# Performance work log

Hardware: AMD Instinct MI355X
Metric: run time of the kernel (lower is better)

Reference implementation:

```python
import jax, jax.numpy as jnp
import numpy as np

B, T, E, H = 16, 4096, 64, 8
K, GADD, RADD, REGION = 256, 8, 8, 64
MIN_SIGMA, SIGMA_SCALE, SIGMA_BOOST = 0.05, 1.0, 2.0
VS = K * (4 + GADD + RADD)


def setup_inputs() -> dict:
    key = jax.random.key(0)
    ks = jax.random.split(key, 10)
    return {
        "x": jax.random.normal(ks[0], (B, T, E), jnp.float32),
        "Wq": jax.random.normal(ks[1], (E, E * H), jnp.float32) / np.float32(np.sqrt(E)),
        "Wk": jax.random.normal(ks[2], (E, E * H), jnp.float32) / np.float32(np.sqrt(E)),
        "Wv": jax.random.normal(ks[3], (E, E * H), jnp.float32) / np.float32(np.sqrt(E)),
        "Wu": jax.random.normal(ks[4], (H * E, E), jnp.float32) / np.float32(np.sqrt(H * E)),
        "bu": jnp.zeros((E,), jnp.float32),
        "means_p": jax.random.normal(ks[5], (K, 2), jnp.float32),
        "sigmas_p": jax.random.normal(ks[6], (K,), jnp.float32),
        "global_ints": jax.random.randint(ks[7], (B, 1, K, GADD, 2), 0, T, jnp.int32),
        "local_offsets": jax.random.randint(ks[8], (B, 1, K, RADD, 2), 0, REGION, jnp.int32),
    }


def _flip(x):
    # util.flip: sort each (i, j) pair so row >= col (below-diagonal / causal)
    hi = jnp.max(x, axis=-1, keepdims=True)
    lo = jnp.min(x, axis=-1, keepdims=True)
    return jnp.concatenate([hi, lo], axis=-1)


def _forward(x, Wq, Wk, Wv, Wu, bu, means_p, sigmas_p, global_ints, local_offsets):
    b, t, e = x.shape
    h, k = H, K

    # ---- hyper(): continuous means/sigmas over the (t, t) attention matrix
    means = jnp.broadcast_to(means_p[None, None], (b, 1, k, 2))
    means = _flip(means)
    means = jax.nn.sigmoid(means) * (t - 1)                       # (b,1,k,2) in [0, t-1]
    sig = jax.nn.softplus(sigmas_p + SIGMA_BOOST) + MIN_SIGMA     # (k,)
    sigmas = jnp.broadcast_to((sig * t * SIGMA_SCALE)[None, None, :, None], (b, 1, k, 2))

    # ---- ngenerate: 2^rank floor/ceil neighbours + global + relative-window samples
    fl, ce = jnp.floor(means), jnp.ceil(means)
    pat = jnp.array([[0., 0.], [0., 1.], [1., 0.], [1., 1.]], jnp.float32)  # (4,2)
    neigh = fl[:, :, :, None, :] * (1.0 - pat) + ce[:, :, :, None, :] * pat
    neigh = jnp.clip(neigh, 0, t - 1).astype(jnp.int32)           # (b,1,k,4,2)
    lower = jnp.clip(jnp.floor(means) - REGION // 2, 0, t - REGION).astype(jnp.int32)
    local = lower[:, :, :, None, :] + local_offsets               # (b,1,k,RADD,2)
    idx = jnp.concatenate([neigh, global_ints, local], axis=3).reshape(b, 1, VS, 2)
    idx = _flip(idx)                                              # (b,1,VS,2), row >= col

    # ---- densities: unnormalized Gaussian weight of each int tuple under each point
    indfl = idx.astype(jnp.float32)
    diff = (indfl[:, :, :, None, :] - means[:, :, None, :, :]) / sigmas[:, :, None, :, :]
    props = jnp.exp(-0.5 * jnp.sum(diff * diff, axis=-1))         # (b,1,VS,K)

    # ---- nduplicates: zero all-but-one of identical index tuples per batch
    ids = idx[:, 0, :, 0] * t + idx[:, 0, :, 1]                   # (b, VS)
    def dupmask(v):
        o = jnp.argsort(v)
        s = v[o]
        d = jnp.concatenate([jnp.zeros((1,), bool), s[1:] == s[:-1]])
        return jnp.zeros((VS,), bool).at[o].set(d)
    dups = jax.vmap(dupmask)(ids)                                  # (b, VS)
    props = jnp.where(dups[:, None, :, None], 0.0, props)
    props = props / jnp.sum(props, axis=2, keepdims=True)
    weights = jnp.sum(props, axis=3)                               # mvalues == 1 -> (b,1,VS)

    # ---- Q/K/V projections, per-head dim = e
    scale = e ** -0.25
    q = (x @ Wq).reshape(b, t, h, e).transpose(0, 2, 1, 3).reshape(b * h, t, e) * scale
    kk = (x @ Wk).reshape(b, t, h, e).transpose(0, 2, 1, 3).reshape(b * h, t, e) * scale
    v = (x @ Wv).reshape(b, t, h, e).transpose(0, 2, 1, 3).reshape(b * h, t, e)

    rows = jnp.broadcast_to(idx[:, 0, None, :, 0], (b, h, VS)).reshape(b * h, VS)
    cols = jnp.broadcast_to(idx[:, 0, None, :, 1], (b, h, VS)).reshape(b * h, VS)
    w = jnp.broadcast_to(weights[:, 0, None, :], (b, h, VS)).reshape(b * h, VS)

    sq = jnp.take_along_axis(q, rows[:, :, None], axis=1)          # (b*h, VS, e)
    sk = jnp.take_along_axis(kk, cols[:, :, None], axis=1)
    dot = w * jnp.sum(sq * sk, axis=-1)                            # (b*h, VS)

    # ---- segment (row-wise) softmax over the sparse pattern
    seg = (jnp.arange(b * h, dtype=jnp.int32)[:, None] * t + rows).reshape(-1)
    dflat = dot.reshape(-1)
    m = jax.lax.stop_gradient(jax.ops.segment_max(dflat, seg, num_segments=b * h * t))
    ex = jnp.exp(dflat - m[seg])
    ssum = jax.ops.segment_sum(ex, seg, num_segments=b * h * t)
    p = ex / ssum[seg]                                             # (b*h*VS,)

    # ---- sparse batched matmul: scatter-add p * V[col] into rows
    gathered = jnp.take_along_axis(v, cols[:, :, None], axis=1).reshape(-1, e)
    out = jax.ops.segment_sum(p[:, None] * gathered, seg, num_segments=b * h * t)
    out = out.reshape(b, h, t, e).transpose(0, 2, 1, 3).reshape(b, t, h * e)
    return out @ Wu + bu


def reference(x, Wq, Wk, Wv, Wu, bu, means_p, sigmas_p, global_ints, local_offsets):
    return _forward(x, Wq, Wk, Wv, Wu, bu, means_p, sigmas_p, global_ints, local_offsets)
```

## Files before the change

### kernel.cpp

```cpp
#include <hip/hip_runtime.h>
#include <hip/hip_bf16.h>
#include <math.h>

#define B 16
#define T 4096
#define E 64
#define H 8
#define KP 256
#define GADD 8
#define RADD 8
#define REGION 64
#define VS (KP * (4 + GADD + RADD))
#define NH (H * E)
#define NCHUNK 20
#define HSZ 16384

typedef __attribute__((ext_vector_type(8))) short bf16x8;
typedef __attribute__((ext_vector_type(4))) float f32x4;

__device__ inline ushort f2bf(float f) {
    union { __hip_bfloat16 h; ushort u; } cv;
    cv.h = __float2bfloat16(f);
    return cv.u;
}
__device__ inline float bflo(uint32_t p) { return __uint_as_float(p << 16); }
__device__ inline float bfhi(uint32_t p) { return __uint_as_float(p & 0xffff0000u); }

__global__ void k_points(const float* __restrict__ means_p, const float* __restrict__ sigmas_p,
                         float* __restrict__ meansf, float* __restrict__ sigt) {
    int k = threadIdx.x;
    if (k >= KP) return;
    float a = means_p[2 * k], b = means_p[2 * k + 1];
    float hi = fmaxf(a, b), lo = fminf(a, b);
    meansf[2 * k]     = (1.f / (1.f + expf(-hi))) * (float)(T - 1);
    meansf[2 * k + 1] = (1.f / (1.f + expf(-lo))) * (float)(T - 1);
    float sp = sigmas_p[k] + 2.0f;
    float s = (sp > 20.f) ? sp : log1pf(expf(sp));
    sigt[k] = (s + 0.05f) * (float)T;
}

__global__ void k_wvu(const float* __restrict__ Wv, const float* __restrict__ Wu,
                      float* __restrict__ Wvu) {
    int idx = blockIdx.x * blockDim.x + threadIdx.x;
    if (idx >= E * NH) return;
    int i = idx / NH, c = idx % NH;
    int h = c / E, j = c % E;
    float acc = 0.f;
    for (int d = 0; d < E; ++d)
        acc += Wv[i * NH + h * E + d] * Wu[(h * E + d) * E + j];
    Wvu[i * NH + c] = acc;
}

__global__ void k_prep_x(const float* __restrict__ x, ushort* __restrict__ xb) {
    int i = (blockIdx.x * 256 + threadIdx.x) * 8;
    float4 a = *(const float4*)(x + i);
    float4 b = *(const float4*)(x + i + 4);
    uint4 r;
    r.x = (uint32_t)f2bf(a.x) | ((uint32_t)f2bf(a.y) << 16);
    r.y = (uint32_t)f2bf(a.z) | ((uint32_t)f2bf(a.w) << 16);
    r.z = (uint32_t)f2bf(b.x) | ((uint32_t)f2bf(b.y) << 16);
    r.w = (uint32_t)f2bf(b.z) | ((uint32_t)f2bf(b.w) << 16);
    *(uint4*)(xb + i) = r;
}

__global__ void k_prep_w(const float* __restrict__ Wq, const float* __restrict__ Wk,
                         const float* __restrict__ Wvu, ushort* __restrict__ wfrag) {
    int t = blockIdx.x * 256 + threadIdx.x;
    if (t >= 3 * 32 * 2 * 64) return;
    int lane = t & 63, kf = (t >> 6) & 1, nf = (t >> 7) & 31, z = t >> 12;
    const float* W = (z == 0) ? Wq : (z == 1) ? Wk : Wvu;
    int col = nf * 16 + (lane & 15);
    int krow = kf * 32 + (lane >> 4) * 8;
    uint4 r;
    uint32_t v[8];
    #pragma unroll
    for (int j = 0; j < 8; ++j) v[j] = f2bf(W[(size_t)(krow + j) * NH + col]);
    r.x = v[0] | (v[1] << 16); r.y = v[2] | (v[3] << 16);
    r.z = v[4] | (v[5] << 16); r.w = v[6] | (v[7] << 16);
    *(uint4*)(wfrag + (size_t)t * 8) = r;
}

__global__ __launch_bounds__(256) void k_proj(const ushort* __restrict__ xb,
        const ushort* __restrict__ wfrag,
        __hip_bfloat16* __restrict__ q, __hip_bfloat16* __restrict__ kk,
        __hip_bfloat16* __restrict__ vu) {
    int z = blockIdx.y;
    __hip_bfloat16* outp = (z == 0) ? q : (z == 1) ? kk : vu;
    int row0 = blockIdx.x * 64;
    int wv = threadIdx.x >> 6, lane = threadIdx.x & 63;
    int arow = lane & 15, akoff = (lane >> 4) * 8;

    bf16x8 bfr[8][2];
    #pragma unroll
    for (int nf = 0; nf < 8; ++nf) {
        size_t base = ((size_t)((z * 32 + wv * 8 + nf) * 2) * 64 + lane) * 8;
        bfr[nf][0] = *(const bf16x8*)(wfrag + base);
        bfr[nf][1] = *(const bf16x8*)(wfrag + base + 64 * 8);
    }

    #pragma unroll
    for (int mf = 0; mf < 4; ++mf) {
        bf16x8 a0 = *(const bf16x8*)(xb + (size_t)(row0 + mf * 16 + arow) * 64 + akoff);
        bf16x8 a1 = *(const bf16x8*)(xb + (size_t)(row0 + mf * 16 + arow) * 64 + 32 + akoff);
        f32x4 acc[8];
        #pragma unroll
        for (int nf = 0; nf < 8; ++nf) {
            f32x4 t = {0.f, 0.f, 0.f, 0.f};
            t = __builtin_amdgcn_mfma_f32_16x16x32_bf16(a0, bfr[nf][0], t, 0, 0, 0);
            t = __builtin_amdgcn_mfma_f32_16x16x32_bf16(a1, bfr[nf][1], t, 0, 0, 0);
            acc[nf] = t;
        }
        int rbase = row0 + mf * 16 + (lane >> 4) * 4;
        #pragma unroll
        for (int rg = 0; rg < 4; ++rg) {
            uint4 o;
            o.x = (uint32_t)f2bf(acc[0][rg]) | ((uint32_t)f2bf(acc[1][rg]) << 16);
            o.y = (uint32_t)f2bf(acc[2][rg]) | ((uint32_t)f2bf(acc[3][rg]) << 16);
            o.z = (uint32_t)f2bf(acc[4][rg]) | ((uint32_t)f2bf(acc[5][rg]) << 16);
            o.w = (uint32_t)f2bf(acc[6][rg]) | ((uint32_t)f2bf(acc[7][rg]) << 16);
            *(uint4*)((ushort*)outp + (size_t)(rbase + rg) * NH + wv * 128 + (lane & 15) * 8) = o;
        }
    }
}

__global__ void k_build_idx(const int* __restrict__ g_ints, const int* __restrict__ l_offs,
                            const float* __restrict__ meansf,
                            int* __restrict__ idxrow, int* __restrict__ idxcol,
                            int* __restrict__ hkey, int* __restrict__ hval) {
    int b = blockIdx.y;
    int s = blockIdx.x * 256 + threadIdx.x;
    int* keys = hkey + b * HSZ;
    int* vals = hval + b * HSZ;
    int k = s / 20, slot = s % 20;
    float m0 = meansf[2 * k], m1 = meansf[2 * k + 1];
    int i0, i1;
    if (slot < 4) {
        float a  = (slot & 2) ? ceilf(m0) : floorf(m0);
        float bb = (slot & 1) ? ceilf(m1) : floorf(m1);
        a  = fminf(fmaxf(a, 0.f), (float)(T - 1));
        bb = fminf(fmaxf(bb, 0.f), (float)(T - 1));
        i0 = (int)a; i1 = (int)bb;
    } else if (slot < 12) {
        const int* p = g_ints + ((size_t)((b * KP + k) * GADD) + (slot - 4)) * 2;
        i0 = p[0]; i1 = p[1];
    } else {
        int lo0 = (int)fminf(fmaxf(floorf(m0) - (float)(REGION / 2), 0.f), (float)(T - REGION));
        int lo1 = (int)fminf(fmaxf(floorf(m1) - (float)(REGION / 2), 0.f), (float)(T - REGION));
        const int* p = l_offs + ((size_t)((b * KP + k) * RADD) + (slot - 12)) * 2;
        i0 = lo0 + p[0]; i1 = lo1 + p[1];
    }
    int row = max(i0, i1), col = min(i0, i1);
    idxrow[b * VS + s] = row;
    idxcol[b * VS + s] = col;
    int id = row * T + col;
    unsigned h = ((unsigned)id * 2654435761u) >> 18;
    while (true) {
        int old = atomicCAS(&keys[h], -1, id);
        if (old == -1 || old == id) { atomicMin(&vals[h], s); break; }
        h = (h + 1) & (HSZ - 1);
    }
}

__global__ __launch_bounds__(256) void k_local(const int* __restrict__ idxrow,
        const int* __restrict__ idxcol, const int* __restrict__ hkey,
        const int* __restrict__ hval, int* __restrict__ lrank, int* __restrict__ dup,
        int* __restrict__ chist) {
    int b = blockIdx.y, chunk = blockIdx.x;
    int tid = threadIdx.x;
    int s = chunk * 256 + tid;
    int r = idxrow[b * VS + s];
    int c = idxcol[b * VS + s];
    __shared__ int srow[256];
    srow[tid] = r;
    __syncthreads();
    int lr = 0;
    #pragma unroll 8
    for (int t = 0; t < 256; ++t) {
        int rt = srow[t];
        lr += (t < tid && rt == r);
    }
    lrank[b * VS + s] = lr;
    atomicAdd(&chist[(size_t)(b * T + r) * NCHUNK + chunk], 1);
    const int* keys = hkey + b * HSZ;
    const int* vals = hval + b * HSZ;
    int id = r * T + c;
    unsigned h = ((unsigned)id * 2654435761u) >> 18;
    while (keys[h] != id) h = (h + 1) & (HSZ - 1);
    dup[b * VS + s] = (vals[h] != s);
}

__global__ void k_chunkscan(int* __restrict__ chist, int* __restrict__ rowcnt) {
    int idx = blockIdx.x * 256 + threadIdx.x;
    int* p = chist + (size_t)idx * NCHUNK;
    int acc = 0;
    #pragma unroll
    for (int c = 0; c < NCHUNK; ++c) { int v = p[c]; p[c] = acc; acc += v; }
    rowcnt[idx] = acc;
}

__global__ void k_colsum(const int* __restrict__ idxrow, const int* __restrict__ idxcol,
                         const int* __restrict__ dup, const float* __restrict__ meansf,
                         const float* __restrict__ sigt, float* __restrict__ colsum) {
    int k = blockIdx.x, b = blockIdx.y;
    float m0 = meansf[2 * k], m1 = meansf[2 * k + 1];
    float inv = 1.f / sigt[k];
    float acc = 0.f;
    for (int s = threadIdx.x; s < VS; s += 256) {
        if (!dup[b * VS + s]) {
            float d0 = ((float)idxrow[b * VS + s] - m0) * inv;
            float d1 = ((float)idxcol[b * VS + s] - m1) * inv;
            acc += __expf(-0.5f * (d0 * d0 + d1 * d1));
        }
    }
    __shared__ float red[256];
    red[threadIdx.x] = acc;
    __syncthreads();
    for (int o = 128; o > 0; o >>= 1) {
        if (threadIdx.x < o) red[threadIdx.x] += red[threadIdx.x + o];
        __syncthreads();
    }
    if (threadIdx.x == 0) colsum[b * KP + k] = red[0];
}

__global__ void k_weights(const int* __restrict__ idxrow, const int* __restrict__ idxcol,
                          const int* __restrict__ dup, const float* __restrict__ meansf,
                          const float* __restrict__ sigt, const float* __restrict__ colsum,
                          float* __restrict__ wts) {
    int b = blockIdx.y;
    int s = blockIdx.x * 256 + threadIdx.x;
    __shared__ float sm[2 * KP], ss[KP], rc[KP];
    for (int k = threadIdx.x; k < KP; k += 256) {
        sm[2 * k] = meansf[2 * k];
        sm[2 * k + 1] = meansf[2 * k + 1];
        ss[k] = 1.f / sigt[k];
        rc[k] = 1.f / colsum[b * KP + k];
    }
    __syncthreads();
    float w = 0.f;
    if (!dup[b * VS + s]) {
        float r = (float)idxrow[b * VS + s], c = (float)idxcol[b * VS + s];
        #pragma unroll 4
        for (int k = 0; k < KP; ++k) {
            float d0 = (r - sm[2 * k]) * ss[k];
            float d1 = (c - sm[2 * k + 1]) * ss[k];
            w += __expf(-0.5f * (d0 * d0 + d1 * d1)) * rc[k];
        }
    }
    wts[b * VS + s] = w;
}

__global__ __launch_bounds__(1024) void k_scan(const int* __restrict__ rowcnt, int* __restrict__ rowptr) {
    int b = blockIdx.x, tid = threadIdx.x;
    __shared__ int part[1024];
    int v[4]; int loc = 0;
    for (int j = 0; j < 4; ++j) { v[j] = rowcnt[b * T + tid * 4 + j]; loc += v[j]; }
    part[tid] = loc;
    __syncthreads();
    for (int off = 1; off < 1024; off <<= 1) {
        int t = (tid >= off) ? part[tid - off] : 0;
        __syncthreads();
        part[tid] += t;
        __syncthreads();
    }
    int excl = part[tid] - loc;
    for (int j = 0; j < 4; ++j) { rowptr[b * (T + 1) + tid * 4 + j] = excl; excl += v[j]; }
    if (tid == 1023) rowptr[b * (T + 1) + T] = part[1023];
}

__global__ void k_scatter(const int* __restrict__ idxrow, const int* __restrict__ idxcol,
                          const float* __restrict__ wts, const int* __restrict__ lrank,
                          const int* __restrict__ chist, const int* __restrict__ rowptr,
                          int* __restrict__ scol, float* __restrict__ sw) {
    int b = blockIdx.y;
    int s = blockIdx.x * 256 + threadIdx.x;
    int r = idxrow[b * VS + s];
    int pos = rowptr[b * (T + 1) + r] + chist[(size_t)(b * T + r) * NCHUNK + (s >> 8)]
            + lrank[b * VS + s];
    scol[b * VS + pos] = idxcol[b * VS + s];
    sw[b * VS + pos] = wts[b * VS + s];
}

__global__ __launch_bounds__(256) void k_attn(
        const __hip_bfloat16* __restrict__ q, const __hip_bfloat16* __restrict__ kk,
        const __hip_bfloat16* __restrict__ vu, const int* __restrict__ rowptr,
        const int* __restrict__ scol, const float* __restrict__ sw,
        const float* __restrict__ bu, float* __restrict__ out) {
    int gr = blockIdx.x * 4 + (threadIdx.x >> 6);
    int b = gr >> 12;
    int r = gr & (T - 1);
    int lane = threadIdx.x & 63;
    int p0 = rowptr[b * (T + 1) + r], p1 = rowptr[b * (T + 1) + r + 1];

    uint4 q4 = *(const uint4*)((const ushort*)q + (size_t)gr * NH + lane * 8);
    float qv[8] = { bflo(q4.x), bfhi(q4.x), bflo(q4.y), bfhi(q4.y),
                    bflo(q4.z), bfhi(q4.z), bflo(q4.w), bfhi(q4.w) };

    float m0 = -INFINITY, s0 = 0.f, m1 = -INFINITY, s1 = 0.f;
    float av[8] = {0.f,0.f,0.f,0.f,0.f,0.f,0.f,0.f};

    for (int e = p0; e < p1; ++e) {
        int c = scol[b * VS + e];
        float w = sw[b * VS + e];
        size_t off = ((size_t)(b * T + c)) * NH + lane * 8;
        uint4 k4 = *(const uint4*)((const ushort*)kk + off);
        float dp0 = qv[0]*bflo(k4.x) + qv[1]*bfhi(k4.x) + qv[2]*bflo(k4.y) + qv[3]*bfhi(k4.y);
        float dp1 = qv[4]*bflo(k4.z) + qv[5]*bfhi(k4.z) + qv[6]*bflo(k4.w) + qv[7]*bfhi(k4.w);
        dp0 += __shfl_xor(dp0, 1);
        dp0 += __shfl_xor(dp0, 2);
        dp0 += __shfl_xor(dp0, 4);
        dp0 += __shfl_xor(dp0, 8);
        dp1 += __shfl_xor(dp1, 1);
        dp1 += __shfl_xor(dp1, 2);
        dp1 += __shfl_xor(dp1, 4);
        dp1 += __shfl_xor(dp1, 8);
        float d0 = 0.125f * w * dp0;
        float d1 = 0.125f * w * dp1;
        uint4 v4 = *(const uint4*)((const ushort*)vu + off);
        float vf[8] = { bflo(v4.x), bfhi(v4.x), bflo(v4.y), bfhi(v4.y),
                        bflo(v4.z), bfhi(v4.z), bflo(v4.w), bfhi(v4.w) };
        float nm0 = fmaxf(m0, d0), c0 = __expf(m0 - nm0), t0 = __expf(d0 - nm0);
        float nm1 = fmaxf(m1, d1), c1 = __expf(m1 - nm1), t1 = __expf(d1 - nm1);
        s0 = s0 * c0 + t0; m0 = nm0;
        s1 = s1 * c1 + t1; m1 = nm1;
        #pragma unroll
        for (int u = 0; u < 4; ++u) av[u] = av[u] * c0 + t0 * vf[u];
        #pragma unroll
        for (int u = 4; u < 8; ++u) av[u] = av[u] * c1 + t1 * vf[u];
    }

    float i0 = (p1 > p0) ? (1.f / s0) : 0.f;
    float i1 = (p1 > p0) ? (1.f / s1) : 0.f;
    float res[4];
    #pragma unroll
    for (int u = 0; u < 4; ++u) {
        float v = av[u] * i0 + av[u + 4] * i1;
        v += __shfl_xor(v, 16);
        v += __shfl_xor(v, 32);
        res[u] = v;
    }
    if (lane < 16) {
        #pragma unroll
        for (int u = 0; u < 4; ++u)
            out[(size_t)gr * E + u * 16 + lane] = res[u] + bu[u * 16 + lane];
    }
}

extern "C" void kernel_launch(void* const* d_in, const int* in_sizes, int n_in,
                              void* d_out, int out_size, void* d_ws, size_t ws_size,
                              hipStream_t stream) {
    const float* x        = (const float*)d_in[0];
    const float* Wq       = (const float*)d_in[1];
    const float* Wk       = (const float*)d_in[2];
    const float* Wv       = (const float*)d_in[3];
    const float* Wu       = (const float*)d_in[4];
    const float* bu       = (const float*)d_in[5];
    const float* means_p  = (const float*)d_in[6];
    const float* sigmas_p = (const float*)d_in[7];
    const int*   g_ints   = (const int*)d_in[8];
    const int*   l_offs   = (const int*)d_in[9];
    float* out = (float*)d_out;

    char* ws = (char*)d_ws;
    size_t o = 0;
    auto alloc = [&](size_t bytes) -> void* {
        void* p = ws + o;
        o += (bytes + 255) & ~(size_t)255;
        return p;
    };
    __hip_bfloat16* q   = (__hip_bfloat16*)alloc((size_t)B * T * NH * 2);
    __hip_bfloat16* kk  = (__hip_bfloat16*)alloc((size_t)B * T * NH * 2);
    __hip_bfloat16* vu  = (__hip_bfloat16*)alloc((size_t)B * T * NH * 2);
    ushort* xb    = (ushort*)alloc((size_t)B * T * E * 2);
    ushort* wfrag = (ushort*)alloc((size_t)3 * 32 * 2 * 64 * 8 * 2);
    float* Wvu    = (float*)alloc((size_t)E * NH * 4);
    float* meansf = (float*)alloc(KP * 2 * 4);
    float* sigt   = (float*)alloc(KP * 4);
    int*   idxrow = (int*)alloc((size_t)B * VS * 4);
    int*   idxcol = (int*)alloc((size_t)B * VS * 4);
    float* wts    = (float*)alloc((size_t)B * VS * 4);
    int*   lrank  = (int*)alloc((size_t)B * VS * 4);
    int*   dup    = (int*)alloc((size_t)B * VS * 4);
    float* colsum = (float*)alloc((size_t)B * KP * 4);
    int*   rowcnt = (int*)alloc((size_t)B * T * 4);
    int*   rowptr = (int*)alloc((size_t)B * (T + 1) * 4);
    int*   scol   = (int*)alloc((size_t)B * VS * 4);
    float* sw     = (float*)alloc((size_t)B * VS * 4);
    int*   hkey   = (int*)alloc((size_t)B * HSZ * 4);
    int*   hval   = (int*)alloc((size_t)B * HSZ * 4);
    int*   chist  = (int*)alloc((size_t)B * T * NCHUNK * 4);

    hipMemsetAsync(hkey, 0xFF, (size_t)B * HSZ * 4, stream);
    hipMemsetAsync(hval, 0x7F, (size_t)B * HSZ * 4, stream);
    hipMemsetAsync(chist, 0, (size_t)B * T * NCHUNK * 4, stream);

    k_points<<<1, 256, 0, stream>>>(means_p, sigmas_p, meansf, sigt);
    k_wvu<<<(E * NH + 255) / 256, 256, 0, stream>>>(Wv, Wu, Wvu);
    k_prep_x<<<(B * T * E / 8) / 256, 256, 0, stream>>>(x, xb);
    k_prep_w<<<(3 * 32 * 2 * 64 + 255) / 256, 256, 0, stream>>>(Wq, Wk, Wvu, wfrag);
    k_build_idx<<<dim3(VS / 256, B), 256, 0, stream>>>(g_ints, l_offs, meansf, idxrow, idxcol, hkey, hval);
    k_local<<<dim3(NCHUNK, B), 256, 0, stream>>>(idxrow, idxcol, hkey, hval, lrank, dup, chist);
    k_chunkscan<<<B * T / 256, 256, 0, stream>>>(chist, rowcnt);
    k_colsum<<<dim3(KP, B), 256, 0, stream>>>(idxrow, idxcol, dup, meansf, sigt, colsum);
    k_weights<<<dim3(VS / 256, B), 256, 0, stream>>>(idxrow, idxcol, dup, meansf, sigt, colsum, wts);
    k_scan<<<B, 1024, 0, stream>>>(rowcnt, rowptr);
    k_scatter<<<dim3(VS / 256, B), 256, 0, stream>>>(idxrow, idxcol, wts, lrank, chist, rowptr, scol, sw);
    k_proj<<<dim3(B * T / 64, 3), 256, 0, stream>>>(xb, wfrag, q, kk, vu);
    k_attn<<<B * T / 4, 256, 0, stream>>>(q, kk, vu, rowptr, scol, sw, bu, out);
}
```

Baseline: 183.7 us.

## Fold Wq into the key projection so attention dots use raw x

Per head, the query-key dot product is reassociated as x_r · (Wq_h Wk_h^T x_c). The combined Wq·Wk^T matrix is precomputed in k_prep_w, so the projection kernel now produces two bf16 outputs (xm and vu) instead of three. The attention kernel reads the fp32 x row directly in place of a projected query. This removes one full B×T×512 bf16 projection write and its read, at the cost of a small per-weight 64-length dot loop in the weight prep kernel and somewhat different rounding, since the product is rounded to bf16 once.

```diff
diff --git a/kernel.cpp b/kernel.cpp
--- a/kernel.cpp
+++ b/kernel.cpp
@@ -66,15 +66,26 @@
 __global__ void k_prep_w(const float* __restrict__ Wq, const float* __restrict__ Wk,
                          const float* __restrict__ Wvu, ushort* __restrict__ wfrag) {
     int t = blockIdx.x * 256 + threadIdx.x;
-    if (t >= 3 * 32 * 2 * 64) return;
+    if (t >= 2 * 32 * 2 * 64) return;
     int lane = t & 63, kf = (t >> 6) & 1, nf = (t >> 7) & 31, z = t >> 12;
-    const float* W = (z == 0) ? Wq : (z == 1) ? Wk : Wvu;
     int col = nf * 16 + (lane & 15);
     int krow = kf * 32 + (lane >> 4) * 8;
+    uint32_t v[8];
+    if (z == 0) {
+        int h = col >> 6, d = col & 63;
+        const float* wqrow = Wq + (size_t)d * NH + h * 64;
+        #pragma unroll
+        for (int j = 0; j < 8; ++j) {
+            const float* wkrow = Wk + (size_t)(krow + j) * NH + h * 64;
+            float acc = 0.f;
+            for (int m = 0; m < 64; ++m) acc += wqrow[m] * wkrow[m];
+            v[j] = f2bf(acc);
+        }
+    } else {
+        #pragma unroll
+        for (int j = 0; j < 8; ++j) v[j] = f2bf(Wvu[(size_t)(krow + j) * NH + col]);
+    }
     uint4 r;
-    uint32_t v[8];
-    #pragma unroll
-    for (int j = 0; j < 8; ++j) v[j] = f2bf(W[(size_t)(krow + j) * NH + col]);
     r.x = v[0] | (v[1] << 16); r.y = v[2] | (v[3] << 16);
     r.z = v[4] | (v[5] << 16); r.w = v[6] | (v[7] << 16);
     *(uint4*)(wfrag + (size_t)t * 8) = r;
@@ -82,10 +93,9 @@
 
 __global__ __launch_bounds__(256) void k_proj(const ushort* __restrict__ xb,
         const ushort* __restrict__ wfrag,
-        __hip_bfloat16* __restrict__ q, __hip_bfloat16* __restrict__ kk,
-        __hip_bfloat16* __restrict__ vu) {
+        __hip_bfloat16* __restrict__ xm, __hip_bfloat16* __restrict__ vu) {
     int z = blockIdx.y;
-    __hip_bfloat16* outp = (z == 0) ? q : (z == 1) ? kk : vu;
+    __hip_bfloat16* outp = (z == 0) ? xm : vu;
     int row0 = blockIdx.x * 64;
     int wv = threadIdx.x >> 6, lane = threadIdx.x & 63;
     int arow = lane & 15, akoff = (lane >> 4) * 8;
@@ -281,7 +291,7 @@
 }
 
 __global__ __launch_bounds__(256) void k_attn(
-        const __hip_bfloat16* __restrict__ q, const __hip_bfloat16* __restrict__ kk,
+        const float* __restrict__ x, const __hip_bfloat16* __restrict__ xm,
         const __hip_bfloat16* __restrict__ vu, const int* __restrict__ rowptr,
         const int* __restrict__ scol, const float* __restrict__ sw,
         const float* __restrict__ bu, float* __restrict__ out) {
@@ -291,9 +301,8 @@
     int lane = threadIdx.x & 63;
     int p0 = rowptr[b * (T + 1) + r], p1 = rowptr[b * (T + 1) + r + 1];
 
-    uint4 q4 = *(const uint4*)((const ushort*)q + (size_t)gr * NH + lane * 8);
-    float qv[8] = { bflo(q4.x), bfhi(q4.x), bflo(q4.y), bfhi(q4.y),
-                    bflo(q4.z), bfhi(q4.z), bflo(q4.w), bfhi(q4.w) };
+    const float* xrow = x + (size_t)gr * E + (lane & 15);
+    float xv0 = xrow[0], xv1 = xrow[16], xv2 = xrow[32], xv3 = xrow[48];
 
     float m0 = -INFINITY, s0 = 0.f, m1 = -INFINITY, s1 = 0.f;
     float av[8] = {0.f,0.f,0.f,0.f,0.f,0.f,0.f,0.f};
@@ -302,9 +311,9 @@
         int c = scol[b * VS + e];
         float w = sw[b * VS + e];
         size_t off = ((size_t)(b * T + c)) * NH + lane * 8;
-        uint4 k4 = *(const uint4*)((const ushort*)kk + off);
-        float dp0 = qv[0]*bflo(k4.x) + qv[1]*bfhi(k4.x) + qv[2]*bflo(k4.y) + qv[3]*bfhi(k4.y);
-        float dp1 = qv[4]*bflo(k4.z) + qv[5]*bfhi(k4.z) + qv[6]*bflo(k4.w) + qv[7]*bfhi(k4.w);
+        uint4 k4 = *(const uint4*)((const ushort*)xm + off);
+        float dp0 = xv0*bflo(k4.x) + xv1*bfhi(k4.x) + xv2*bflo(k4.y) + xv3*bfhi(k4.y);
+        float dp1 = xv0*bflo(k4.z) + xv1*bfhi(k4.z) + xv2*bflo(k4.w) + xv3*bfhi(k4.w);
         dp0 += __shfl_xor(dp0, 1);
         dp0 += __shfl_xor(dp0, 2);
         dp0 += __shfl_xor(dp0, 4);
@@ -367,11 +376,10 @@
         o += (bytes + 255) & ~(size_t)255;
         return p;
     };
-    __hip_bfloat16* q   = (__hip_bfloat16*)alloc((size_t)B * T * NH * 2);
-    __hip_bfloat16* kk  = (__hip_bfloat16*)alloc((size_t)B * T * NH * 2);
+    __hip_bfloat16* xm  = (__hip_bfloat16*)alloc((size_t)B * T * NH * 2);
     __hip_bfloat16* vu  = (__hip_bfloat16*)alloc((size_t)B * T * NH * 2);
     ushort* xb    = (ushort*)alloc((size_t)B * T * E * 2);
-    ushort* wfrag = (ushort*)alloc((size_t)3 * 32 * 2 * 64 * 8 * 2);
+    ushort* wfrag = (ushort*)alloc((size_t)2 * 32 * 2 * 64 * 8 * 2);
     float* Wvu    = (float*)alloc((size_t)E * NH * 4);
     float* meansf = (float*)alloc(KP * 2 * 4);
     float* sigt   = (float*)alloc(KP * 4);
@@ -396,7 +404,7 @@
     k_points<<<1, 256, 0, stream>>>(means_p, sigmas_p, meansf, sigt);
     k_wvu<<<(E * NH + 255) / 256, 256, 0, stream>>>(Wv, Wu, Wvu);
     k_prep_x<<<(B * T * E / 8) / 256, 256, 0, stream>>>(x, xb);
-    k_prep_w<<<(3 * 32 * 2 * 64 + 255) / 256, 256, 0, stream>>>(Wq, Wk, Wvu, wfrag);
+    k_prep_w<<<(2 * 32 * 2 * 64 + 255) / 256, 256, 0, stream>>>(Wq, Wk, Wvu, wfrag);
     k_build_idx<<<dim3(VS / 256, B), 256, 0, stream>>>(g_ints, l_offs, meansf, idxrow, idxcol, hkey, hval);
     k_local<<<dim3(NCHUNK, B), 256, 0, stream>>>(idxrow, idxcol, hkey, hval, lrank, dup, chist);
     k_chunkscan<<<B * T / 256, 256, 0, stream>>>(chist, rowcnt);
@@ -404,6 +412,6 @@
     k_weights<<<dim3(VS / 256, B), 256, 0, stream>>>(idxrow, idxcol, dup, meansf, sigt, colsum, wts);
     k_scan<<<B, 1024, 0, stream>>>(rowcnt, rowptr);
     k_scatter<<<dim3(VS / 256, B), 256, 0, stream>>>(idxrow, idxcol, wts, lrank, chist, rowptr, scol, sw);
-    k_proj<<<dim3(B * T / 64, 3), 256, 0, stream>>>(xb, wfrag, q, kk, vu);
-    k_attn<<<B * T / 4, 256, 0, stream>>>(q, kk, vu, rowptr, scol, sw, bu, out);
-}
+    k_proj<<<dim3(B * T / 64, 2), 256, 0, stream>>>(xb, wfrag, xm, vu);
+    k_attn<<<B * T / 4, 256, 0, stream>>>(x, xm, vu, rowptr, scol, sw, bu, out);
+}
```

Result: slower. 188.8 us (+2.8%).
